# Kernel tuning notes

Measured on AMD Instinct MI355X. Metric: run time of the kernel, lower is better.

Reference implementation:

```python
import jax, jax.numpy as jnp
import numpy as np
import math

# Model hyperparameters (SchNet defaults)
H = 128        # hidden_channels
F = 128        # num_filters
G = 50         # num_gaussians
CUT = 6.0      # cutoff (Angstrom)
L_INT = 3      # num_interactions
# Graph scale
N_MOL = 512    # molecules
APM = 32       # atoms per molecule
N = N_MOL * APM
BOX = 10.0     # side of cubic box per molecule


def _ssp(x):
    # ShiftedSoftplus
    return jax.nn.softplus(x) - math.log(2.0)


def setup_inputs() -> dict:
    rng = np.random.default_rng(0)
    pos = rng.uniform(0.0, BOX, (N_MOL, APM, 3)).astype(np.float32)
    # radius graph within each molecule (faithful to radius_graph_custom,
    # precomputed here because edge count is data-dependent)
    srcs, dsts = [], []
    for m in range(N_MOL):
        p = pos[m]
        dm = np.linalg.norm(p[:, None, :] - p[None, :, :], axis=-1)
        mask = dm <= CUT
        np.fill_diagonal(mask, False)
        s, t = np.nonzero(mask)
        srcs.append(s + m * APM)
        dsts.append(t + m * APM)
    edge_index = np.stack([np.concatenate(srcs), np.concatenate(dsts)]).astype(np.int32)
    pos = pos.reshape(N, 3)
    batch = np.repeat(np.arange(N_MOL, dtype=np.int32), APM)
    z = rng.integers(1, 100, N).astype(np.int32)

    key = jax.random.key(0)
    ks = jax.random.split(key, 16)
    s = 0.1
    nrm = lambda k, shp: (jax.random.normal(k, shp, dtype=jnp.float32) * s)
    return {
        "z": jnp.asarray(z),
        "pos": jnp.asarray(pos),
        "batch": jnp.asarray(batch),
        "edge_index": jnp.asarray(edge_index),
        "emb": nrm(ks[0], (100, H)),
        "mlp_w1": nrm(ks[1], (L_INT, G, F)),
        "mlp_b1": jnp.zeros((L_INT, F), jnp.float32),
        "mlp_w2": nrm(ks[2], (L_INT, F, F)),
        "mlp_b2": jnp.zeros((L_INT, F), jnp.float32),
        "cf1_w": nrm(ks[3], (L_INT, H, F)),
        "cf2_w": nrm(ks[4], (L_INT, F, H)),
        "cf2_b": jnp.zeros((L_INT, H), jnp.float32),
        "lin_w": nrm(ks[5], (L_INT, H, H)),
        "lin_b": jnp.zeros((L_INT, H), jnp.float32),
        "out1_w": nrm(ks[6], (H, H // 2)),
        "out1_b": jnp.zeros((H // 2,), jnp.float32),
        "out2_w": nrm(ks[7], (H // 2, 1)),
        "out2_b": jnp.zeros((1,), jnp.float32),
    }


def reference(z, pos, batch, edge_index, emb,
              mlp_w1, mlp_b1, mlp_w2, mlp_b2,
              cf1_w, cf2_w, cf2_b, lin_w, lin_b,
              out1_w, out1_b, out2_w, out2_b):
    src, dst = edge_index[0], edge_index[1]
    # edge_weight = euclidean distance (== cdist[src, dst])
    d = jnp.sqrt(jnp.sum((pos[src] - pos[dst]) ** 2, axis=-1))  # [E]
    # GaussianSmearing
    offs = jnp.linspace(0.0, CUT, G)
    coeff = -0.5 / (CUT / (G - 1)) ** 2
    edge_attr = jnp.exp(coeff * (d[:, None] - offs[None, :]) ** 2)  # [E, G]
    # cosine cutoff
    Ccut = 0.5 * (jnp.cos(d * math.pi / CUT) + 1.0)  # [E]

    h = emb[z]  # [N, H]
    for l in range(L_INT):
        # edge filter MLP with cutoff
        W = _ssp(edge_attr @ mlp_w1[l] + mlp_b1[l]) @ mlp_w2[l] + mlp_b2[l]  # [E, F]
        W = W * Ccut[:, None]
        # CFConv: lin1 -> gather x_j -> multiply -> scatter-add to dst -> lin2
        msg = (h @ cf1_w[l])[src] * W                                # [E, F]
        agg = jax.ops.segment_sum(msg, dst, num_segments=N)          # [N, F]
        v = agg @ cf2_w[l] + cf2_b[l]                                # [N, H]
        v = _ssp(v)
        v = v @ lin_w[l] + lin_b[l]
        h = h + v  # residual

    h = _ssp(h @ out1_w + out1_b)
    h = h @ out2_w + out2_b                                          # [N, 1]
    out = jax.ops.segment_sum(h, batch, num_segments=N_MOL)          # [N_MOL, 1]
    return out
```

## Files before the change

kernel.cpp:

```cpp
#include <hip/hip_runtime.h>
#include <hip/hip_bf16.h>
#include <math.h>

#define NATOMS 16384
#define NMOL   512
#define APM    32
#define GDIM   50
#define KTAB   4096

#define STRH 132
#define STRA 136

typedef __attribute__((ext_vector_type(8))) short   short8;
typedef __attribute__((ext_vector_type(4))) float   floatx4;

__device__ __forceinline__ float ssp(float x) {
    float e = __expf(-fabsf(x));
    return fmaxf(x, 0.0f) + __logf(1.0f + e) - 0.69314718055994531f;
}

__device__ __forceinline__ unsigned short f2bf(float x) {
    union { float f; unsigned int u; } v; v.f = x;
    unsigned int lsb = (v.u >> 16) & 1u;
    v.u += 0x7fffu + lsb;
    return (unsigned short)(v.u >> 16);
}

__device__ __forceinline__ unsigned int pk2bf(float a, float b) {
    __hip_bfloat162 h = __float22bfloat162_rn(make_float2(a, b));
    unsigned int u;
    __builtin_memcpy(&u, &h, 4);
    return u;
}

#define KW1 72
#define KW2 136
#define NTILE (KTAB / 64)

__global__ __launch_bounds__(256) void mega_setup_kernel(
    const float* __restrict__ pos, const int* __restrict__ eidx, int E, int EB,
    int* __restrict__ rowptr,
    const float* __restrict__ cf1, const float* __restrict__ cf2,
    const float* __restrict__ lin, const float* __restrict__ out1,
    unsigned short* __restrict__ Wtall, unsigned int* __restrict__ meta,
    const float* __restrict__ w1_, const float* __restrict__ b1_,
    const float* __restrict__ w2_, const float* __restrict__ b2_,
    unsigned short* __restrict__ Tt)
{
    const int WB = (9 * 16384 + 64 * 128 + 255) / 256;
    const int b = blockIdx.x;
    const int tid = threadIdx.x;

    if (b < EB) {
        int idx = b * 256 + tid;
        if (idx < E) {
            int s = eidx[idx], t = eidx[E + idx];
            float dx = pos[3 * s]     - pos[3 * t];
            float dy = pos[3 * s + 1] - pos[3 * t + 1];
            float dz = pos[3 * s + 2] - pos[3 * t + 2];
            float d  = sqrtf(dx * dx + dy * dy + dz * dz);
            float u  = d * (float)(KTAB - 1) / 6.0f;
            int i = min((int)(u + 0.5f), KTAB - 1);
            meta[idx] = ((unsigned)i << 10) | ((unsigned)(s & 31) << 5) | (unsigned)(t & 31);
        } else if (idx < E + NATOMS + 1) {
            int a = idx - E;
            int lo = 0, hi = E;
            while (lo < hi) { int mid = (lo + hi) >> 1; if (eidx[mid] < a) lo = mid + 1; else hi = mid; }
            rowptr[a] = lo;
        }
        return;
    }
    if (b < EB + WB) {
        int idx = (b - EB) * 256 + tid;
        if (idx < 9 * 16384) {
            int wi = idx >> 14, rem = idx & 16383;
            int n = rem >> 7, k = rem & 127;
            int l = wi / 3, which = wi % 3;
            const float* src = (which == 0) ? cf1 : (which == 1) ? cf2 : lin;
            Wtall[idx] = f2bf(src[(size_t)l * 16384 + k * 128 + n]);
        } else if (idx < 9 * 16384 + 64 * 128) {
            int q = idx - 9 * 16384;
            int n = q >> 7, k = q & 127;
            Wtall[idx] = f2bf(out1[k * 64 + n]);
        }
        return;
    }

    __shared__ unsigned short s_bufA[128 * KW2];
    __shared__ unsigned short s_bufB[128 * KW1];

    const int tt = b - EB - WB;
    const int l  = tt / NTILE;
    const int bx = tt % NTILE;
    const float* w1 = w1_ + (size_t)l * GDIM * 128;
    const float* b1 = b1_ + (size_t)l * 128;
    const float* w2 = w2_ + (size_t)l * 128 * 128;
    const float* b2 = b2_ + (size_t)l * 128;
    unsigned short* Tg = Tt + (size_t)l * KTAB * 128;

    unsigned short* s_w1T = s_bufB;
    unsigned short* s_w2T = s_bufA;
    unsigned short* s_t   = s_bufB;

    for (int i = tid; i < GDIM * 128; i += 256) {
        int g = i >> 7, f = i & 127;
        s_w1T[f * KW1 + g] = f2bf(w1[i]);
    }
    for (int i = tid; i < (64 - GDIM) * 128; i += 256) {
        int g = GDIM + (i >> 7), f = i & 127;
        s_w1T[f * KW1 + g] = 0;
    }
    for (int i = tid; i < 128 * 128; i += 256) {
        int k = i >> 7, n = i & 127;
        s_w2T[n * KW2 + k] = f2bf(w2[i]);
    }

    const int lane = tid & 63;
    const int w    = tid >> 6;
    const int l15  = lane & 15;
    const int quad = lane >> 4;

    float b1v[8], b2v[8];
    #pragma unroll
    for (int nt = 0; nt < 8; nt++) {
        b1v[nt] = b1[nt * 16 + l15];
        b2v[nt] = b2[nt * 16 + l15];
    }
    __syncthreads();

    const float hstep = 6.0f / (float)(KTAB - 1);
    const float step  = 6.0f / 49.0f;
    const float coeff = -0.5f / (step * step);
    const float pioc  = 3.14159265358979323846f / 6.0f;
    const int k0 = bx * 64;
    const float dm = (float)(k0 + w * 16 + l15) * hstep;

    floatx4 acc1[8];
    #pragma unroll
    for (int nt = 0; nt < 8; nt++) acc1[nt] = (floatx4){0.f, 0.f, 0.f, 0.f};
    #pragma unroll
    for (int ks = 0; ks < 2; ks++) {
        unsigned int ap[4];
        #pragma unroll
        for (int jj = 0; jj < 4; jj++) {
            int g0 = ks * 32 + quad * 8 + 2 * jj;
            float d0 = dm - (float)g0 * step;
            float d1 = dm - (float)(g0 + 1) * step;
            float v0 = (g0 < GDIM)     ? __expf(coeff * d0 * d0) : 0.0f;
            float v1 = (g0 + 1 < GDIM) ? __expf(coeff * d1 * d1) : 0.0f;
            ap[jj] = pk2bf(v0, v1);
        }
        short8 af;
        __builtin_memcpy(&af, ap, 16);
        #pragma unroll
        for (int nt = 0; nt < 8; nt++) {
            short8 bfg = *(const short8*)&s_w1T[(nt * 16 + l15) * KW1 + ks * 32 + quad * 8];
            acc1[nt] = __builtin_amdgcn_mfma_f32_16x16x32_bf16(af, bfg, acc1[nt], 0, 0, 0);
        }
    }
    __syncthreads();

    #pragma unroll
    for (int nt = 0; nt < 8; nt++) {
        #pragma unroll
        for (int r = 0; r < 4; r++) {
            int row = w * 16 + quad * 4 + r;
            s_t[row * KW2 + nt * 16 + l15] = f2bf(ssp(acc1[nt][r] + b1v[nt]));
        }
    }

    floatx4 acc2[8];
    #pragma unroll
    for (int nt = 0; nt < 8; nt++) acc2[nt] = (floatx4){0.f, 0.f, 0.f, 0.f};
    #pragma unroll
    for (int ks = 0; ks < 4; ks++) {
        short8 af = *(const short8*)&s_t[(w * 16 + l15) * KW2 + ks * 32 + quad * 8];
        #pragma unroll
        for (int nt = 0; nt < 8; nt++) {
            short8 bfg = *(const short8*)&s_w2T[(nt * 16 + l15) * KW2 + ks * 32 + quad * 8];
            acc2[nt] = __builtin_amdgcn_mfma_f32_16x16x32_bf16(af, bfg, acc2[nt], 0, 0, 0);
        }
    }

    #pragma unroll
    for (int nt = 0; nt < 8; nt++) {
        #pragma unroll
        for (int r = 0; r < 4; r++) {
            int row = w * 16 + quad * 4 + r;
            float d = (float)(k0 + row) * hstep;
            float cut = 0.5f * (__cosf(d * pioc) + 1.0f);
            Tg[(size_t)(k0 + row) * 128 + nt * 16 + l15] = f2bf((acc2[nt][r] + b2v[nt]) * cut);
        }
    }
}

__global__ __launch_bounds__(512, 4) void fused_schnet_kernel(
    const int* __restrict__ z, const float* __restrict__ emb,
    const int* __restrict__ rowptr, const unsigned int* __restrict__ meta,
    const unsigned short* __restrict__ Tt,
    const unsigned short* __restrict__ Wtall,
    const float* __restrict__ cf2_b, const float* __restrict__ lin_b,
    const float* __restrict__ out1_b, const float* __restrict__ out2_w,
    const float* __restrict__ out2_b,
    float* __restrict__ out)
{
    __shared__ float s_h[32 * STRH];
    __shared__ float s_hx[33 * 128];
    __shared__ unsigned short s_agg[32 * STRA];
    __shared__ uint2 s_meta2[32 * 32];
    __shared__ float s_red;
    unsigned short* s_t = (unsigned short*)s_hx;

    const int tid  = threadIdx.x;
    const int lane = tid & 63;
    const int w    = tid >> 6;
    const int l15  = lane & 15;
    const int quad = lane >> 4;
    const int r16  = (w & 1) * 16;
    const int c32  = (w >> 1) * 32;
    const int B0   = blockIdx.x * 32;

    const int half = lane >> 5;
    const int l31  = lane & 31;
    const unsigned tOff = (unsigned)(l31 << 3);
    const unsigned hOff = (unsigned)(l31 << 4);

    for (int i = tid; i < 32 * 128; i += 512) {
        int row = i >> 7, col = i & 127;
        s_h[row * STRH + col] = emb[(size_t)z[B0 + row] * 128 + col];
    }
    if (tid < 128) s_hx[32 * 128 + tid] = 0.0f;
    if (tid == 0) s_red = 0.0f;
    for (int i = tid; i < 32 * 32; i += 512)
        s_meta2[i] = make_uint2(0u, 32u << 9);

    const int ebase = rowptr[B0];
    const int nE    = rowptr[B0 + 32] - ebase;

    __syncthreads();

    for (int i = tid; i < nE; i += 512) {
        unsigned q = meta[ebase + i];
        int a = (int)((q >> 5) & 31u);
        int slot = i - (rowptr[B0 + a] - ebase);
        s_meta2[(a << 5) + slot] = make_uint2((q >> 10) << 8, (q & 31u) << 9);
    }

    const int rp = rowptr[B0 + w * 4 + min(lane, 4)] - ebase;

    const unsigned short* WtO = Wtall + 9 * 16384;
    const char* hxB = (const char*)s_hx;

    for (int l = 0; l < 3; l++) {
        const unsigned short* W1 = Wtall + (size_t)(l * 3 + 0) * 16384;
        const unsigned short* W2 = Wtall + (size_t)(l * 3 + 1) * 16384;
        const unsigned short* W3 = Wtall + (size_t)(l * 3 + 2) * 16384;
        const char* TlB = (const char*)(Tt + (size_t)l * KTAB * 128);

        __syncthreads();

        floatx4 acc[2];
        #pragma unroll
        for (int nt = 0; nt < 2; nt++) acc[nt] = (floatx4){0.f, 0.f, 0.f, 0.f};
        #pragma unroll
        for (int ks = 0; ks < 4; ks++) {
            const float* hp = &s_h[(r16 + l15) * STRH + ks * 32 + quad * 8];
            float4 xa = *(const float4*)hp;
            float4 xb = *(const float4*)(hp + 4);
            unsigned int ap[4];
            ap[0] = pk2bf(xa.x, xa.y); ap[1] = pk2bf(xa.z, xa.w);
            ap[2] = pk2bf(xb.x, xb.y); ap[3] = pk2bf(xb.z, xb.w);
            short8 af;
            __builtin_memcpy(&af, ap, 16);
            #pragma unroll
            for (int nt = 0; nt < 2; nt++) {
                short8 bfg = *(const short8*)&W1[(size_t)(c32 + nt * 16 + l15) * 128 + ks * 32 + quad * 8];
                acc[nt] = __builtin_amdgcn_mfma_f32_16x16x32_bf16(af, bfg, acc[nt], 0, 0, 0);
            }
        }
        #pragma unroll
        for (int nt = 0; nt < 2; nt++) {
            #pragma unroll
            for (int r = 0; r < 4; r++)
                s_hx[(r16 + quad * 4 + r) * 128 + c32 + nt * 16 + l15] = acc[nt][r];
        }

        __syncthreads();

        for (int al = 0; al < 4; al++) {
            const int atom = w * 4 + al;
            const int deg  = __shfl(rp, al + 1) - __shfl(rp, al);
            const uint2* mp = &s_meta2[(atom << 5) + half];
            float pa[4][4];
            #pragma unroll
            for (int j = 0; j < 4; j++) {
                #pragma unroll
                for (int c = 0; c < 4; c++) pa[j][c] = 0.0f;
            }
            const int nb = (deg + 7) >> 3;
            for (int bb = 0; bb < nb; bb++) {
                #pragma unroll
                for (int j = 0; j < 4; j++) {
                    uint2 m  = mp[(bb << 3) + (j << 1)];
                    uint2 tp = *(const uint2*)(TlB + (m.x + tOff));
                    float4 hv = *(const float4*)(hxB + (m.y + hOff));
                    pa[j][0] = fmaf(hv.x, __uint_as_float(tp.x << 16),         pa[j][0]);
                    pa[j][1] = fmaf(hv.y, __uint_as_float(tp.x & 0xffff0000u), pa[j][1]);
                    pa[j][2] = fmaf(hv.z, __uint_as_float(tp.y << 16),         pa[j][2]);
                    pa[j][3] = fmaf(hv.w, __uint_as_float(tp.y & 0xffff0000u), pa[j][3]);
                }
            }
            float c0 = (pa[0][0] + pa[1][0]) + (pa[2][0] + pa[3][0]);
            float c1 = (pa[0][1] + pa[1][1]) + (pa[2][1] + pa[3][1]);
            float c2 = (pa[0][2] + pa[1][2]) + (pa[2][2] + pa[3][2]);
            float c3 = (pa[0][3] + pa[1][3]) + (pa[2][3] + pa[3][3]);
            c0 += __shfl_xor(c0, 32);
            c1 += __shfl_xor(c1, 32);
            c2 += __shfl_xor(c2, 32);
            c3 += __shfl_xor(c3, 32);
            if (half == 0) {
                uint2 pk = make_uint2(pk2bf(c0, c1), pk2bf(c2, c3));
                *(uint2*)&s_agg[atom * STRA + (l31 << 2)] = pk;
            }
        }

        __syncthreads();

        float bva[2], bvb[2];
        #pragma unroll
        for (int nt = 0; nt < 2; nt++) {
            bva[nt] = cf2_b[l * 128 + c32 + nt * 16 + l15];
            bvb[nt] = lin_b[l * 128 + c32 + nt * 16 + l15];
        }
        #pragma unroll
        for (int nt = 0; nt < 2; nt++) acc[nt] = (floatx4){0.f, 0.f, 0.f, 0.f};
        #pragma unroll
        for (int ks = 0; ks < 4; ks++) {
            short8 af = *(const short8*)&s_agg[(r16 + l15) * STRA + ks * 32 + quad * 8];
            #pragma unroll
            for (int nt = 0; nt < 2; nt++) {
                short8 bfg = *(const short8*)&W2[(size_t)(c32 + nt * 16 + l15) * 128 + ks * 32 + quad * 8];
                acc[nt] = __builtin_amdgcn_mfma_f32_16x16x32_bf16(af, bfg, acc[nt], 0, 0, 0);
            }
        }
        #pragma unroll
        for (int nt = 0; nt < 2; nt++) {
            #pragma unroll
            for (int r = 0; r < 4; r++) {
                int row = r16 + quad * 4 + r;
                s_t[row * STRA + c32 + nt * 16 + l15] = f2bf(ssp(acc[nt][r] + bva[nt]));
            }
        }

        __syncthreads();

        #pragma unroll
        for (int nt = 0; nt < 2; nt++) acc[nt] = (floatx4){0.f, 0.f, 0.f, 0.f};
        #pragma unroll
        for (int ks = 0; ks < 4; ks++) {
            short8 af = *(const short8*)&s_t[(r16 + l15) * STRA + ks * 32 + quad * 8];
            #pragma unroll
            for (int nt = 0; nt < 2; nt++) {
                short8 bfg = *(const short8*)&W3[(size_t)(c32 + nt * 16 + l15) * 128 + ks * 32 + quad * 8];
                acc[nt] = __builtin_amdgcn_mfma_f32_16x16x32_bf16(af, bfg, acc[nt], 0, 0, 0);
            }
        }
        #pragma unroll
        for (int nt = 0; nt < 2; nt++) {
            #pragma unroll
            for (int r = 0; r < 4; r++) {
                int row = r16 + quad * 4 + r;
                s_h[row * STRH + c32 + nt * 16 + l15] += acc[nt][r] + bvb[nt];
            }
        }
    }

    __syncthreads();

    const int c16 = (w >> 1) * 16;
    floatx4 ha = (floatx4){0.f, 0.f, 0.f, 0.f};
    #pragma unroll
    for (int ks = 0; ks < 4; ks++) {
        const float* hp = &s_h[(r16 + l15) * STRH + ks * 32 + quad * 8];
        float4 xa = *(const float4*)hp;
        float4 xb = *(const float4*)(hp + 4);
        unsigned int ap[4];
        ap[0] = pk2bf(xa.x, xa.y); ap[1] = pk2bf(xa.z, xa.w);
        ap[2] = pk2bf(xb.x, xb.y); ap[3] = pk2bf(xb.z, xb.w);
        short8 af;
        __builtin_memcpy(&af, ap, 16);
        short8 bfg = *(const short8*)&WtO[(size_t)(c16 + l15) * 128 + ks * 32 + quad * 8];
        ha = __builtin_amdgcn_mfma_f32_16x16x32_bf16(af, bfg, ha, 0, 0, 0);
    }
    float part = 0.0f;
    {
        float b1o = out1_b[c16 + l15];
        float o2  = out2_w[c16 + l15];
        #pragma unroll
        for (int r = 0; r < 4; r++)
            part += ssp(ha[r] + b1o) * o2;
    }
    #pragma unroll
    for (int off = 32; off > 0; off >>= 1) part += __shfl_down(part, off);
    if (lane == 0) atomicAdd(&s_red, part);
    __syncthreads();
    if (tid == 0) out[blockIdx.x] = s_red + 32.0f * out2_b[0];
}

extern "C" void kernel_launch(void* const* d_in, const int* in_sizes, int n_in,
                              void* d_out, int out_size, void* d_ws, size_t ws_size,
                              hipStream_t stream)
{
    const int*   z      = (const int*)d_in[0];
    const float* pos    = (const float*)d_in[1];
    const int*   eidx   = (const int*)d_in[3];
    const float* emb    = (const float*)d_in[4];
    const float* mlp_w1 = (const float*)d_in[5];
    const float* mlp_b1 = (const float*)d_in[6];
    const float* mlp_w2 = (const float*)d_in[7];
    const float* mlp_b2 = (const float*)d_in[8];
    const float* cf1_w  = (const float*)d_in[9];
    const float* cf2_w  = (const float*)d_in[10];
    const float* cf2_b  = (const float*)d_in[11];
    const float* lin_w  = (const float*)d_in[12];
    const float* lin_b  = (const float*)d_in[13];
    const float* out1_w = (const float*)d_in[14];
    const float* out1_b = (const float*)d_in[15];
    const float* out2_w = (const float*)d_in[16];
    const float* out2_b = (const float*)d_in[17];
    const int E = in_sizes[3] / 2;

    char* p = (char*)d_ws;
    unsigned int* meta = (unsigned int*)p;        p += ((size_t)(E + 1) * 4 + 63) & ~63ULL;
    unsigned short* Tt = (unsigned short*)p;      p += (size_t)3 * KTAB * 128 * 2;
    int* rowptr = (int*)p;                        p += ((size_t)(NATOMS + 1) * 4 + 63) & ~63ULL;
    unsigned short* Wtall = (unsigned short*)p;

    const int EB = (E + NATOMS + 1 + 255) / 256;
    const int WB = (9 * 16384 + 64 * 128 + 255) / 256;
    const int TB = NTILE * 3;
    mega_setup_kernel<<<EB + WB + TB, 256, 0, stream>>>(
        pos, eidx, E, EB, rowptr, cf1_w, cf2_w, lin_w, out1_w, Wtall, meta,
        mlp_w1, mlp_b1, mlp_w2, mlp_b2, Tt);

    fused_schnet_kernel<<<NMOL, 512, 0, stream>>>(
        z, emb, rowptr, meta, Tt, Wtall,
        cf2_b, lin_b, out1_b, out2_w, out2_b, (float*)d_out);
}
```

Baseline: 178.2 us.

## Replace per-atom edge lists with dense 32x32 pair-indexed filter offsets and zero row

Edge metadata moves from compacted per-destination lists of (table offset, source offset) pairs into a dense 32x32 array indexed by (dst, src). Missing pairs point at a new zeroed extra row in the filter table. The aggregation loop becomes a fixed, fully unrolled 16-step loop per half-wave, with source h addresses computed rather than loaded. This removes degree-dependent loop bounds, rowptr shuffles and the per-edge slot computation, at the cost of always processing all 32 pairs even when degree is smaller.

```diff
diff --git a/kernel.cpp b/kernel.cpp
--- a/kernel.cpp
+++ b/kernel.cpp
@@ -67,6 +67,10 @@
             int lo = 0, hi = E;
             while (lo < hi) { int mid = (lo + hi) >> 1; if (eidx[mid] < a) lo = mid + 1; else hi = mid; }
             rowptr[a] = lo;
+        } else if (idx < E + NATOMS + 1 + 3 * 128) {
+            int q = idx - (E + NATOMS + 1);
+            int l = q >> 7, f = q & 127;
+            Tt[(size_t)l * (KTAB + 1) * 128 + (size_t)KTAB * 128 + f] = 0;
         }
         return;
     }
@@ -96,7 +100,7 @@
     const float* b1 = b1_ + (size_t)l * 128;
     const float* w2 = w2_ + (size_t)l * 128 * 128;
     const float* b2 = b2_ + (size_t)l * 128;
-    unsigned short* Tg = Tt + (size_t)l * KTAB * 128;
+    unsigned short* Tg = Tt + (size_t)l * (KTAB + 1) * 128;
 
     unsigned short* s_w1T = s_bufB;
     unsigned short* s_w2T = s_bufA;
@@ -205,9 +209,9 @@
     float* __restrict__ out)
 {
     __shared__ float s_h[32 * STRH];
-    __shared__ float s_hx[33 * 128];
+    __shared__ float s_hx[32 * 128];
     __shared__ unsigned short s_agg[32 * STRA];
-    __shared__ uint2 s_meta2[32 * 32];
+    __shared__ unsigned int s_ko[32 * 32];
     __shared__ float s_red;
     unsigned short* s_t = (unsigned short*)s_hx;
 
@@ -229,10 +233,9 @@
         int row = i >> 7, col = i & 127;
         s_h[row * STRH + col] = emb[(size_t)z[B0 + row] * 128 + col];
     }
-    if (tid < 128) s_hx[32 * 128 + tid] = 0.0f;
     if (tid == 0) s_red = 0.0f;
     for (int i = tid; i < 32 * 32; i += 512)
-        s_meta2[i] = make_uint2(0u, 32u << 9);
+        s_ko[i] = (unsigned)(KTAB << 8);
 
     const int ebase = rowptr[B0];
     const int nE    = rowptr[B0 + 32] - ebase;
@@ -241,12 +244,9 @@
 
     for (int i = tid; i < nE; i += 512) {
         unsigned q = meta[ebase + i];
-        int a = (int)((q >> 5) & 31u);
-        int slot = i - (rowptr[B0 + a] - ebase);
-        s_meta2[(a << 5) + slot] = make_uint2((q >> 10) << 8, (q & 31u) << 9);
-    }
-
-    const int rp = rowptr[B0 + w * 4 + min(lane, 4)] - ebase;
+        int dstA = q & 31, srcA = (q >> 5) & 31;
+        s_ko[(dstA << 5) + ((srcA & 1) << 4) + (srcA >> 1)] = (q >> 10) << 8;
+    }
 
     const unsigned short* WtO = Wtall + 9 * 16384;
     const char* hxB = (const char*)s_hx;
@@ -255,7 +255,7 @@
         const unsigned short* W1 = Wtall + (size_t)(l * 3 + 0) * 16384;
         const unsigned short* W2 = Wtall + (size_t)(l * 3 + 1) * 16384;
         const unsigned short* W3 = Wtall + (size_t)(l * 3 + 2) * 16384;
-        const char* TlB = (const char*)(Tt + (size_t)l * KTAB * 128);
+        const char* TlB = (const char*)(Tt + (size_t)l * (KTAB + 1) * 128);
 
         __syncthreads();
 
@@ -288,27 +288,32 @@
         __syncthreads();
 
         for (int al = 0; al < 4; al++) {
-            const int atom = w * 4 + al;
-            const int deg  = __shfl(rp, al + 1) - __shfl(rp, al);
-            const uint2* mp = &s_meta2[(atom << 5) + half];
+            const int atom = (w << 2) + al;
+            const unsigned* ko = &s_ko[(atom << 5) + (half << 4)];
+            uint4 k0 = *(const uint4*)&ko[0];
+            uint4 k1 = *(const uint4*)&ko[4];
+            uint4 k2 = *(const uint4*)&ko[8];
+            uint4 k3 = *(const uint4*)&ko[12];
+            const unsigned koff[16] = { k0.x, k0.y, k0.z, k0.w,
+                                        k1.x, k1.y, k1.z, k1.w,
+                                        k2.x, k2.y, k2.z, k2.w,
+                                        k3.x, k3.y, k3.z, k3.w };
             float pa[4][4];
             #pragma unroll
             for (int j = 0; j < 4; j++) {
                 #pragma unroll
                 for (int c = 0; c < 4; c++) pa[j][c] = 0.0f;
             }
-            const int nb = (deg + 7) >> 3;
-            for (int bb = 0; bb < nb; bb++) {
-                #pragma unroll
-                for (int j = 0; j < 4; j++) {
-                    uint2 m  = mp[(bb << 3) + (j << 1)];
-                    uint2 tp = *(const uint2*)(TlB + (m.x + tOff));
-                    float4 hv = *(const float4*)(hxB + (m.y + hOff));
-                    pa[j][0] = fmaf(hv.x, __uint_as_float(tp.x << 16),         pa[j][0]);
-                    pa[j][1] = fmaf(hv.y, __uint_as_float(tp.x & 0xffff0000u), pa[j][1]);
-                    pa[j][2] = fmaf(hv.z, __uint_as_float(tp.y << 16),         pa[j][2]);
-                    pa[j][3] = fmaf(hv.w, __uint_as_float(tp.y & 0xffff0000u), pa[j][3]);
-                }
+            #pragma unroll
+            for (int stp = 0; stp < 16; stp++) {
+                const int pr = (stp << 1) + half;
+                uint2 tp = *(const uint2*)(TlB + (koff[stp] + tOff));
+                float4 hv = *(const float4*)(hxB + (unsigned)(pr << 9) + hOff);
+                const int j = stp & 3;
+                pa[j][0] = fmaf(hv.x, __uint_as_float(tp.x << 16),         pa[j][0]);
+                pa[j][1] = fmaf(hv.y, __uint_as_float(tp.x & 0xffff0000u), pa[j][1]);
+                pa[j][2] = fmaf(hv.z, __uint_as_float(tp.y << 16),         pa[j][2]);
+                pa[j][3] = fmaf(hv.w, __uint_as_float(tp.y & 0xffff0000u), pa[j][3]);
             }
             float c0 = (pa[0][0] + pa[1][0]) + (pa[2][0] + pa[3][0]);
             float c1 = (pa[0][1] + pa[1][1]) + (pa[2][1] + pa[3][1]);
@@ -432,11 +437,11 @@
 
     char* p = (char*)d_ws;
     unsigned int* meta = (unsigned int*)p;        p += ((size_t)(E + 1) * 4 + 63) & ~63ULL;
-    unsigned short* Tt = (unsigned short*)p;      p += (size_t)3 * KTAB * 128 * 2;
+    unsigned short* Tt = (unsigned short*)p;      p += (size_t)3 * (KTAB + 1) * 128 * 2;
     int* rowptr = (int*)p;                        p += ((size_t)(NATOMS + 1) * 4 + 63) & ~63ULL;
     unsigned short* Wtall = (unsigned short*)p;
 
-    const int EB = (E + NATOMS + 1 + 255) / 256;
+    const int EB = (E + NATOMS + 1 + 3 * 128 + 255) / 256;
     const int WB = (9 * 16384 + 64 * 128 + 255) / 256;
     const int TB = NTILE * 3;
     mega_setup_kernel<<<EB + WB + TB, 256, 0, stream>>>(
```

New measurement: 170.0 us. 1.05x faster.
